# Kernel tuning notes

Hardware: AMD Instinct MI355X
Metric: run time of the kernel (lower is better)

Reference implementation:

```python
import jax, jax.numpy as jnp
import numpy as np

B, T, D, H = 16384, 80, 12, 128


def setup_inputs() -> dict:
    key = jax.random.key(0)
    ks = jax.random.split(key, 20)
    stdv = lambda n: 1.0 / np.sqrt(n)
    u = lambda k, shp, s: jax.random.uniform(k, shp, jnp.float32, -s, s)
    inp = {
        'values': jax.random.normal(ks[0], (B, T, D), jnp.float32),
        'masks': (jax.random.uniform(ks[1], (B, T, D)) < 0.8).astype(jnp.float32),
        'deltas': jax.random.uniform(ks[2], (B, T, D), jnp.float32, 0.0, 5.0),
        'td_h_W': u(ks[3], (H, D), stdv(H)), 'td_h_b': u(ks[4], (H,), stdv(H)),
        'td_x_W': u(ks[5], (D, D), stdv(D)), 'td_x_b': u(ks[6], (D,), stdv(D)),
        'hist_W': u(ks[7], (D, H), stdv(H)), 'hist_b': u(ks[8], (D,), stdv(H)),
        'feat_W': u(ks[9], (D, D), stdv(D)), 'feat_b': u(ks[10], (D,), stdv(D)),
        'wc_W': u(ks[11], (D, 2 * D), stdv(2 * D)), 'wc_b': u(ks[12], (D,), stdv(2 * D)),
        'W_ih': u(ks[13], (4 * H, 2 * D), stdv(H)), 'b_ih': u(ks[14], (4 * H,), stdv(H)),
        'W_hh': u(ks[15], (4 * H, H), stdv(H)), 'b_hh': u(ks[16], (4 * H,), stdv(H)),
        'out_W': u(ks[17], (1, H), stdv(H)), 'out_b': u(ks[18], (1,), stdv(H)),
    }
    return inp


def _forward(values, masks, deltas, td_h_W, td_h_b, td_x_W, td_x_b,
             hist_W, hist_b, feat_W, feat_b, wc_W, wc_b,
             W_ih, b_ih, W_hh, b_hh, out_W, out_b):
    eye = jnp.eye(D, dtype=values.dtype)
    td_x_Wd = td_x_W * eye            # diagonal temporal decay
    feat_Wm = feat_W * (1.0 - eye)

    xs = (jnp.swapaxes(values, 0, 1),  # [T,B,D]
          jnp.swapaxes(masks, 0, 1),
          jnp.swapaxes(deltas, 0, 1))

    def step(carry, xmd):
        h, c, x_loss = carry
        x, m, d = xmd
        gamma_h = jnp.exp(-jax.nn.relu(d @ td_h_W.T + td_h_b))   # [B,H]
        gamma_x = jnp.exp(-jax.nn.relu(d @ td_x_Wd.T + td_x_b))  # [B,D]
        h = h * gamma_h
        x_h = h @ hist_W.T + hist_b
        denom = jnp.sum(m) + 1e-5
        x_loss += jnp.sum(jnp.abs(x - x_h) * m) / denom
        x_c = m * x + (1.0 - m) * x_h
        z_h = x_c @ feat_Wm.T + feat_b
        x_loss += jnp.sum(jnp.abs(x - z_h) * m) / denom
        alpha = jnp.concatenate([gamma_x, m], axis=1) @ wc_W.T + wc_b
        c_h = alpha * z_h + (1.0 - alpha) * x_h
        x_loss += jnp.sum(jnp.abs(x - c_h) * m) / denom
        c_c = m * x + (1.0 - m) * c_h
        inp = jnp.concatenate([c_c, m], axis=1)                  # [B,2D]
        gates = inp @ W_ih.T + b_ih + h @ W_hh.T + b_hh          # [B,4H]
        i, f, g, o = jnp.split(gates, 4, axis=1)
        c = jax.nn.sigmoid(f) * c + jax.nn.sigmoid(i) * jnp.tanh(g)
        h = jax.nn.sigmoid(o) * jnp.tanh(c)
        return (h, c, x_loss), c_c

    h0 = jnp.zeros((values.shape[0], H), values.dtype)
    c0 = jnp.zeros((values.shape[0], H), values.dtype)
    (h, c, x_loss), imps = jax.lax.scan(step, (h0, c0, jnp.float32(0.0)), xs)
    loss = x_loss / T
    predictions = jax.nn.sigmoid(h @ out_W.T + out_b)            # [B,1]
    imputations = jnp.swapaxes(imps, 0, 1)                       # [B,T,D]
    return loss, predictions, imputations


def reference(values, masks, deltas, td_h_W, td_h_b, td_x_W, td_x_b,
              hist_W, hist_b, feat_W, feat_b, wc_W, wc_b,
              W_ih, b_ih, W_hh, b_hh, out_W, out_b):
    return _forward(values, masks, deltas, td_h_W, td_h_b, td_x_W, td_x_b,
                    hist_W, hist_b, feat_W, feat_b, wc_W, wc_b,
                    W_ih, b_ih, W_hh, b_hh, out_W, out_b)
```

## Files before the change

### kernel.cpp

```cpp
#include <hip/hip_runtime.h>

#define B_ 16384
#define T_ 80
#define D_ 12
#define H_ 128
#define BT 32
#define NTH 512
#define NBLK (B_ / BT)

#define NLOG2E -1.4426950408889634f
#define TWOLOG2E 2.8853900817779268f

typedef unsigned short us_t;
typedef unsigned int u32_t;
typedef short bf16x8 __attribute__((ext_vector_type(8)));
typedef float f32x4 __attribute__((ext_vector_type(4)));

__device__ __forceinline__ us_t f2bf_bit(float f){
  u32_t x = __float_as_uint(f);
  return (us_t)((x + 0x7FFFu + ((x >> 16) & 1u)) >> 16);
}
__device__ __forceinline__ us_t f2bf(float f){
  u32_t r;
  asm("v_cvt_pk_bf16_f32 %0, %1, %2" : "=v"(r) : "v"(f), "v"(f));
  return (us_t)r;
}
__device__ __forceinline__ float bf2f(us_t u){
  union { u32_t i; float f; } v; v.i = ((u32_t)u) << 16; return v.f;
}
__device__ __forceinline__ float rcpf(float x){ return __builtin_amdgcn_rcpf(x); }
#if __has_builtin(__builtin_amdgcn_exp2f)
__device__ __forceinline__ float exp2f_(float x){ return __builtin_amdgcn_exp2f(x); }
#else
__device__ __forceinline__ float exp2f_(float x){ return __expf(0.6931471805599453f * x); }
#endif
__device__ __forceinline__ float sigm(float x){ return rcpf(1.f + __expf(-x)); }

__global__ void k_denom(const float* __restrict__ masks, float* __restrict__ denomInv) {
  int t = blockIdx.x, tid = threadIdx.x;
  float s = 0.f;
  for (int b = tid; b < B_; b += 256) {
    const float4* p = (const float4*)(masks + ((size_t)b * T_ + t) * D_);
    float4 a = p[0], c = p[1], d = p[2];
    s += a.x + a.y + a.z + a.w + c.x + c.y + c.z + c.w + d.x + d.y + d.z + d.w;
  }
  __shared__ float r[256];
  r[tid] = s; __syncthreads();
  for (int st = 128; st > 0; st >>= 1) { if (tid < st) r[tid] += r[tid + st]; __syncthreads(); }
  if (tid == 0) denomInv[t] = 1.f / (r[0] + 1e-5f);
}

__global__ void k_pack(const float* __restrict__ W_ih, const float* __restrict__ W_hh,
                       const float* __restrict__ hist_W, const float* __restrict__ td_h_W,
                       const float* __restrict__ b_ih, const float* __restrict__ b_hh,
                       const float* __restrict__ wc_W,
                       us_t* __restrict__ Wb, us_t* __restrict__ histB,
                       us_t* __restrict__ tdhwB, float* __restrict__ bias_pk,
                       us_t* __restrict__ wcB) {
  int idx = blockIdx.x * 256 + threadIdx.x;
  if (idx < 81920) {
    int i = idx & 7, lane = (idx >> 3) & 63, rest = idx >> 9;
    int kc = rest % 5; rest /= 5;
    int g = rest & 3, w = rest >> 2;
    int n = g * 128 + w * 16 + (lane & 15);
    int k = kc * 32 + ((lane >> 4) << 3) + i;
    float v = 0.f;
    if (k < 24) v = W_ih[n * 24 + k];
    else if (k < 152) v = W_hh[n * 128 + (k - 24)];
    float s = (g == 2) ? TWOLOG2E : NLOG2E;
    Wb[idx] = f2bf_bit(v * s);
  } else if (idx < 83968) {
    int e = idx - 81920;
    int i = e & 7, lane = (e >> 3) & 63, kc = e >> 9;
    int col = lane & 15, k = kc * 32 + ((lane >> 4) << 3) + i;
    histB[e] = f2bf_bit(col < 12 ? hist_W[col * 128 + k] : 0.f);
  } else if (idx < 88064) {
    int e = idx - 83968;
    int i = e & 7, lane = (e >> 3) & 63, w = e >> 9;
    int n = w * 16 + (lane & 15), k = ((lane >> 4) << 3) + i;
    tdhwB[e] = f2bf_bit(k < 12 ? td_h_W[n * 12 + k] * NLOG2E : 0.f);
  } else if (idx < 88576) {
    int e = idx - 88064;
    int g = e >> 7;
    float s = (g == 2) ? TWOLOG2E : NLOG2E;
    bias_pk[e] = (b_ih[e] + b_hh[e]) * s;
  } else if (idx < 89088) {
    int e = idx - 88576;
    int i = e & 7, lane = e >> 3;
    int col = lane & 15, k = ((lane >> 4) << 3) + i;
    wcB[e] = f2bf_bit((col < 12 && k < 24) ? wc_W[col * 24 + k] : 0.f);
  }
}

#define STAGE_WRITE(BUF, V) do { \
  if (la == 0) { \
    x_s[BUF][lb][lq*4+0] = (V).x; x_s[BUF][lb][lq*4+1] = (V).y; \
    x_s[BUF][lb][lq*4+2] = (V).z; x_s[BUF][lb][lq*4+3] = (V).w; \
  } else if (la == 1) { \
    m_s[BUF][lb][lq*4+0] = (V).x; m_s[BUF][lb][lq*4+1] = (V).y; \
    m_s[BUF][lb][lq*4+2] = (V).z; m_s[BUF][lb][lq*4+3] = (V).w; \
    float _mv[4] = {(V).x,(V).y,(V).z,(V).w}; \
    _Pragma("unroll") \
    for (int _j = 0; _j < 4; ++_j) { \
      int _k = 12 + lq*4 + _j; \
      us_t _mb = f2bf(_mv[_j]); \
      A_s[BUF][_k>>3][lb][_k&7] = _mb; \
      aA_s[_k>>3][lb][_k&7] = _mb; \
    } \
  } else { \
    float _dv[4] = {(V).x,(V).y,(V).z,(V).w}; \
    _Pragma("unroll") \
    for (int _j = 0; _j < 4; ++_j) { \
      int _i = lq*4+_j; \
      float _gx = exp2f_(fminf(fmaf(_dv[_j], tdxd_s[_i], tdxb_s[_i]), 0.f)); \
      aA_s[_i>>3][lb][_i&7] = f2bf(_gx); \
      dA_s[_i>>3][lb][_i&7] = f2bf(_dv[_j]); \
    } \
  } \
} while(0)

__global__ __launch_bounds__(NTH) void k_main(
    const float* __restrict__ values, const float* __restrict__ masks, const float* __restrict__ deltas,
    const float* __restrict__ td_h_b, const float* __restrict__ td_x_W, const float* __restrict__ td_x_b,
    const float* __restrict__ hist_b, const float* __restrict__ feat_W, const float* __restrict__ feat_b,
    const float* __restrict__ wc_b,
    const float* __restrict__ out_W, const float* __restrict__ out_b,
    const float* __restrict__ denomInv, const float* __restrict__ bias_pk,
    const us_t* __restrict__ Wb, const us_t* __restrict__ histB, const us_t* __restrict__ tdhwB,
    const us_t* __restrict__ wcB,
    float* __restrict__ blockLoss, float* __restrict__ out_pred, float* __restrict__ out_imp) {

  __shared__ __align__(16) us_t A_s[2][20][BT][8];
  __shared__ __align__(16) us_t dA_s[4][BT][8];
  __shared__ __align__(16) us_t aA_s[4][BT][8];
  __shared__ __align__(16) us_t histB_s[4][64][8];
  __shared__ float x_s[2][BT][13], m_s[2][BT][13];
  __shared__ float cct_s[BT][13], xh_s[BT][13], al_s[BT][13];
  __shared__ float featW_s[12][12];
  __shared__ float featb_s[12], tdxd_s[12], tdxb_s[12];
  __shared__ float outW_s[128];
  __shared__ float denomInv_s[80];
  __shared__ float outb_s;
  __shared__ float red_s[NTH];

  const int tid = threadIdx.x;
  const int bs = blockIdx.x * BT;
  const int w = tid >> 6, l = tid & 63;
  const int lr = l & 15, lg = l >> 4;

  for (int i = tid; i < 144; i += NTH)
    featW_s[i / 12][i % 12] = ((i / 12) == (i % 12)) ? 0.f : feat_W[i];
  if (tid < 12) {
    featb_s[tid] = feat_b[tid];
    tdxd_s[tid] = td_x_W[tid * 12 + tid] * NLOG2E;
    tdxb_s[tid] = td_x_b[tid] * NLOG2E;
  }
  if (tid < 128) outW_s[tid] = out_W[tid];
  if (tid < 80) denomInv_s[tid] = denomInv[tid];
  if (tid == 0) outb_s = out_b[0];
  for (int i = tid; i < 2 * 20 * BT * 8; i += NTH) ((us_t*)A_s)[i] = 0;
  for (int i = tid; i < 4 * BT * 8; i += NTH) { ((us_t*)dA_s)[i] = 0; ((us_t*)aA_s)[i] = 0; }
  for (int i = tid; i < 2048; i += NTH) ((us_t*)histB_s)[i] = histB[i];

  bf16x8 bq[4][5];
  #pragma unroll
  for (int g = 0; g < 4; ++g)
    #pragma unroll
    for (int kc = 0; kc < 5; ++kc)
      bq[g][kc] = *(const bf16x8*)(Wb + (size_t)((((w * 4 + g) * 5 + kc) * 64 + l) << 3));
  const bf16x8 twf = *(const bf16x8*)(tdhwB + (size_t)(((w * 64) + l) << 3));
  const bf16x8 wcf = *(const bf16x8*)(wcB + (size_t)(l << 3));
  float bjs[4];
  #pragma unroll
  for (int g = 0; g < 4; ++g) bjs[g] = bias_pk[g * 128 + w * 16 + lr];
  const float tdhb_j = td_h_b[w * 16 + lr] * NLOG2E;
  const float hbias = hist_b[lr < 12 ? lr : 0];
  const float wcb_lr = (lr < 12) ? wc_b[lr] : 0.f;

  const int lt = tid - 192;
  const bool isLoader = (lt >= 0 && lt < 288);
  const int la = isLoader ? lt / 96 : 0;
  const int lrm = isLoader ? lt % 96 : 0;
  const int lb = lrm / 3, lq = lrm % 3;
  const float* lsrc = (la == 0) ? values : (la == 1) ? masks : deltas;

  float c_st[2][4] = {{0.f,0.f,0.f,0.f},{0.f,0.f,0.f,0.f}};
  float lossAcc = 0.f;
  int cur = 0;
  __syncthreads();

  if (isLoader) {
    float4 pv = *(const float4*)(lsrc + ((size_t)(bs + lb) * T_) * D_ + lq * 4);
    STAGE_WRITE(0, pv);
  }
  __syncthreads();

  for (int t = 0; t < T_; ++t) {
    const float dInv = denomInv_s[t];
    const int nxt = cur ^ 1;
    float4 ldv;

    if (w < 2) {
      f32x4 xacc = {0.f, 0.f, 0.f, 0.f};
      #pragma unroll
      for (int kc = 0; kc < 4; ++kc) {
        const bf16x8 af = *(const bf16x8*)&A_s[cur][3 + kc * 4 + lg][w * 16 + lr][0];
        const bf16x8 hf = *(const bf16x8*)&histB_s[kc][l][0];
        xacc = __builtin_amdgcn_mfma_f32_16x16x32_bf16(af, hf, xacc, 0, 0, 0);
      }
      if (lr < 12) {
        #pragma unroll
        for (int r = 0; r < 4; ++r) xh_s[w * 16 + lg * 4 + r][lr] = xacc[r] + hbias;
      }
    } else if (w == 2) {
      f32x4 ac0 = {wcb_lr, wcb_lr, wcb_lr, wcb_lr};
      f32x4 ac1 = ac0;
      const bf16x8 a0 = *(const bf16x8*)&aA_s[lg][lr][0];
      const bf16x8 a1 = *(const bf16x8*)&aA_s[lg][16 + lr][0];
      ac0 = __builtin_amdgcn_mfma_f32_16x16x32_bf16(a0, wcf, ac0, 0, 0, 0);
      ac1 = __builtin_amdgcn_mfma_f32_16x16x32_bf16(a1, wcf, ac1, 0, 0, 0);
      if (lr < 12) {
        #pragma unroll
        for (int r = 0; r < 4; ++r) {
          al_s[lg * 4 + r][lr] = ac0[r];
          al_s[16 + lg * 4 + r][lr] = ac1[r];
        }
      }
    } else if (isLoader) {
      if (t + 1 < T_)
        ldv = *(const float4*)(lsrc + ((size_t)(bs + lb) * T_ + (t + 1)) * D_ + lq * 4);
    } else if (t > 0) {
      int ib = tid - 480;
      #pragma unroll
      for (int q = 0; q < 3; ++q) {
        float4 v = make_float4(cct_s[ib][q * 4 + 0], cct_s[ib][q * 4 + 1],
                               cct_s[ib][q * 4 + 2], cct_s[ib][q * 4 + 3]);
        *(float4*)(out_imp + ((size_t)(bs + ib) * T_ + (t - 1)) * D_ + q * 4) = v;
      }
    }
    __syncthreads();

    if (isLoader && (t + 1 < T_)) STAGE_WRITE(nxt, ldv);
    if (tid < 384) {
      int b = tid & 31, i = tid >> 5;
      float xh = xh_s[b][i], xv = x_s[cur][b][i], mv = m_s[cur][b][i];
      float es = fabsf(xv - xh) * mv;
      float zh = featb_s[i];
      #pragma unroll
      for (int k = 0; k < 12; ++k) {
        float xck = fmaf(m_s[cur][b][k], x_s[cur][b][k] - xh_s[b][k], xh_s[b][k]);
        zh = fmaf(xck, featW_s[i][k], zh);
      }
      es += fabsf(xv - zh) * mv;
      float al = al_s[b][i];
      float ch = fmaf(al, zh - xh, xh);
      es += fabsf(xv - ch) * mv;
      lossAcc = fmaf(es, dInv, lossAcc);
      float cc = fmaf(mv, xv - ch, ch);
      cct_s[b][i] = cc;
      A_s[cur][i >> 3][b][i & 7] = f2bf(cc);
    }
    __syncthreads();

    {
      f32x4 acc[2][4];
      #pragma unroll
      for (int m = 0; m < 2; ++m)
        #pragma unroll
        for (int g = 0; g < 4; ++g)
          acc[m][g] = (f32x4){bjs[g], bjs[g], bjs[g], bjs[g]};
      __builtin_amdgcn_s_setprio(1);
      #pragma unroll
      for (int kc = 0; kc < 5; ++kc) {
        const bf16x8 a0 = *(const bf16x8*)&A_s[cur][kc * 4 + lg][lr][0];
        const bf16x8 a1 = *(const bf16x8*)&A_s[cur][kc * 4 + lg][16 + lr][0];
        #pragma unroll
        for (int g = 0; g < 4; ++g) {
          acc[0][g] = __builtin_amdgcn_mfma_f32_16x16x32_bf16(a0, bq[g][kc], acc[0][g], 0, 0, 0);
          acc[1][g] = __builtin_amdgcn_mfma_f32_16x16x32_bf16(a1, bq[g][kc], acc[1][g], 0, 0, 0);
        }
      }
      f32x4 g0 = {tdhb_j, tdhb_j, tdhb_j, tdhb_j};
      f32x4 g1 = g0;
      const bf16x8 d0 = *(const bf16x8*)&dA_s[lg][lr][0];
      const bf16x8 d1 = *(const bf16x8*)&dA_s[lg][16 + lr][0];
      g0 = __builtin_amdgcn_mfma_f32_16x16x32_bf16(d0, twf, g0, 0, 0, 0);
      g1 = __builtin_amdgcn_mfma_f32_16x16x32_bf16(d1, twf, g1, 0, 0, 0);
      __builtin_amdgcn_s_setprio(0);
      const bool dec = (t + 1 < T_);
      const int kgh = 3 + 2 * w + (lr >> 3), pgh = lr & 7;
      #pragma unroll
      for (int m = 0; m < 2; ++m) {
        #pragma unroll
        for (int r = 0; r < 4; ++r) {
          float gi = rcpf(1.f + exp2f_(acc[m][0][r]));
          float gf = rcpf(1.f + exp2f_(acc[m][1][r]));
          float gg = 1.f - 2.f * rcpf(1.f + exp2f_(acc[m][2][r]));
          float go = rcpf(1.f + exp2f_(acc[m][3][r]));
          float c = fmaf(gf, c_st[m][r], gi * gg);
          c_st[m][r] = c;
          float th = 1.f - 2.f * rcpf(1.f + exp2f_(TWOLOG2E * c));
          float pre = (m == 0 ? g0[r] : g1[r]);
          float gh = dec ? exp2f_(fminf(pre, 0.f)) : 1.f;
          A_s[nxt][kgh][m * 16 + lg * 4 + r][pgh] = f2bf(go * th * gh);
        }
      }
    }
    __syncthreads();
    cur = nxt;
  }

  if (tid >= 480) {
    int ib = tid - 480;
    #pragma unroll
    for (int q = 0; q < 3; ++q) {
      float4 v = make_float4(cct_s[ib][q * 4 + 0], cct_s[ib][q * 4 + 1],
                             cct_s[ib][q * 4 + 2], cct_s[ib][q * 4 + 3]);
      *(float4*)(out_imp + ((size_t)(bs + ib) * T_ + (T_ - 1)) * D_ + q * 4) = v;
    }
  }

  if (tid < BT) {
    float a = outb_s;
    #pragma unroll 4
    for (int k = 0; k < H_; ++k)
      a = fmaf(bf2f(A_s[cur][3 + (k >> 3)][tid][k & 7]), outW_s[k], a);
    out_pred[bs + tid] = sigm(a);
  }

  red_s[tid] = lossAcc;
  __syncthreads();
  for (int s = NTH / 2; s > 0; s >>= 1) { if (tid < s) red_s[tid] += red_s[tid + s]; __syncthreads(); }
  if (tid == 0) blockLoss[blockIdx.x] = red_s[0];
}

__global__ void k_final(const float* __restrict__ blockLoss, float* __restrict__ out_loss) {
  __shared__ float r[256];
  int tid = threadIdx.x;
  r[tid] = blockLoss[tid] + blockLoss[tid + 256];
  __syncthreads();
  for (int s = 128; s > 0; s >>= 1) { if (tid < s) r[tid] += r[tid + s]; __syncthreads(); }
  if (tid == 0) out_loss[0] = r[0] * (1.f / (float)T_);
}

extern "C" void kernel_launch(void* const* d_in, const int* in_sizes, int n_in,
                              void* d_out, int out_size, void* d_ws, size_t ws_size,
                              hipStream_t stream) {
  const float* values = (const float*)d_in[0];
  const float* masks  = (const float*)d_in[1];
  const float* deltas = (const float*)d_in[2];
  const float* td_h_W = (const float*)d_in[3];
  const float* td_h_b = (const float*)d_in[4];
  const float* td_x_W = (const float*)d_in[5];
  const float* td_x_b = (const float*)d_in[6];
  const float* hist_W = (const float*)d_in[7];
  const float* hist_b = (const float*)d_in[8];
  const float* feat_W = (const float*)d_in[9];
  const float* feat_b = (const float*)d_in[10];
  const float* wc_W   = (const float*)d_in[11];
  const float* wc_b   = (const float*)d_in[12];
  const float* W_ih   = (const float*)d_in[13];
  const float* b_ih   = (const float*)d_in[14];
  const float* W_hh   = (const float*)d_in[15];
  const float* b_hh   = (const float*)d_in[16];
  const float* out_W  = (const float*)d_in[17];
  const float* out_b  = (const float*)d_in[18];

  float* ws_f      = (float*)d_ws;
  float* denomInv  = ws_f;
  float* bias_pk   = ws_f + 128;
  float* blockLoss = ws_f + 1024;
  us_t* Wb    = (us_t*)(ws_f + 2048);
  us_t* histB = Wb + 81920;
  us_t* tdhwB = histB + 2048;
  us_t* wcB   = tdhwB + 4096;

  float* out_f = (float*)d_out;

  k_denom<<<T_, 256, 0, stream>>>(masks, denomInv);
  k_pack<<<348, 256, 0, stream>>>(W_ih, W_hh, hist_W, td_h_W, b_ih, b_hh, wc_W,
                                  Wb, histB, tdhwB, bias_pk, wcB);
  k_main<<<NBLK, NTH, 0, stream>>>(values, masks, deltas, td_h_b, td_x_W, td_x_b,
                                   hist_b, feat_W, feat_b, wc_b,
                                   out_W, out_b, denomInv, bias_pk, Wb, histB, tdhwB, wcB,
                                   blockLoss, out_f + 1, out_f + 1 + B_);
  k_final<<<1, 256, 0, stream>>>(blockLoss, out_f);
}
```

Baseline: 458.5 us.

## Process two 32-row batch tiles per block to amortize per-step syncs

Doubles the batch tile from 32 to 64 rows per block by giving every shared-memory buffer and the cell state a tile dimension, then looping each pipeline stage over the two 32-row sub-tiles. This halves the grid to 256 blocks and spreads the per-timestep barrier and weight-register setup over twice the work. The cost is fewer blocks than CUs on a 256-CU part, longer serial work per step, and more shared memory and registers, which can lower occupancy. The final loss reduction is adjusted to read 256 block partials.

```diff
diff --git a/kernel.cpp b/kernel.cpp
--- a/kernel.cpp
+++ b/kernel.cpp
@@ -4,7 +4,7 @@
 #define T_ 80
 #define D_ 12
 #define H_ 128
-#define BT 32
+#define BT 64
 #define NTH 512
 #define NBLK (B_ / BT)
 
@@ -92,20 +92,20 @@
   }
 }
 
-#define STAGE_WRITE(BUF, V) do { \
+#define STAGE_WRITE(TL, BUF, V) do { \
   if (la == 0) { \
-    x_s[BUF][lb][lq*4+0] = (V).x; x_s[BUF][lb][lq*4+1] = (V).y; \
-    x_s[BUF][lb][lq*4+2] = (V).z; x_s[BUF][lb][lq*4+3] = (V).w; \
+    x_s[TL][BUF][lb][lq*4+0] = (V).x; x_s[TL][BUF][lb][lq*4+1] = (V).y; \
+    x_s[TL][BUF][lb][lq*4+2] = (V).z; x_s[TL][BUF][lb][lq*4+3] = (V).w; \
   } else if (la == 1) { \
-    m_s[BUF][lb][lq*4+0] = (V).x; m_s[BUF][lb][lq*4+1] = (V).y; \
-    m_s[BUF][lb][lq*4+2] = (V).z; m_s[BUF][lb][lq*4+3] = (V).w; \
+    m_s[TL][BUF][lb][lq*4+0] = (V).x; m_s[TL][BUF][lb][lq*4+1] = (V).y; \
+    m_s[TL][BUF][lb][lq*4+2] = (V).z; m_s[TL][BUF][lb][lq*4+3] = (V).w; \
     float _mv[4] = {(V).x,(V).y,(V).z,(V).w}; \
     _Pragma("unroll") \
     for (int _j = 0; _j < 4; ++_j) { \
       int _k = 12 + lq*4 + _j; \
       us_t _mb = f2bf(_mv[_j]); \
-      A_s[BUF][_k>>3][lb][_k&7] = _mb; \
-      aA_s[_k>>3][lb][_k&7] = _mb; \
+      A_s[TL][BUF][_k>>3][lb][_k&7] = _mb; \
+      aA_s[TL][_k>>3][lb][_k&7] = _mb; \
     } \
   } else { \
     float _dv[4] = {(V).x,(V).y,(V).z,(V).w}; \
@@ -113,8 +113,8 @@
     for (int _j = 0; _j < 4; ++_j) { \
       int _i = lq*4+_j; \
       float _gx = exp2f_(fminf(fmaf(_dv[_j], tdxd_s[_i], tdxb_s[_i]), 0.f)); \
-      aA_s[_i>>3][lb][_i&7] = f2bf(_gx); \
-      dA_s[_i>>3][lb][_i&7] = f2bf(_dv[_j]); \
+      aA_s[TL][_i>>3][lb][_i&7] = f2bf(_gx); \
+      dA_s[TL][_i>>3][lb][_i&7] = f2bf(_dv[_j]); \
     } \
   } \
 } while(0)
@@ -130,12 +130,12 @@
     const us_t* __restrict__ wcB,
     float* __restrict__ blockLoss, float* __restrict__ out_pred, float* __restrict__ out_imp) {
 
-  __shared__ __align__(16) us_t A_s[2][20][BT][8];
-  __shared__ __align__(16) us_t dA_s[4][BT][8];
-  __shared__ __align__(16) us_t aA_s[4][BT][8];
+  __shared__ __align__(16) us_t A_s[2][2][20][32][8];
+  __shared__ __align__(16) us_t dA_s[2][4][32][8];
+  __shared__ __align__(16) us_t aA_s[2][4][32][8];
   __shared__ __align__(16) us_t histB_s[4][64][8];
-  __shared__ float x_s[2][BT][13], m_s[2][BT][13];
-  __shared__ float cct_s[BT][13], xh_s[BT][13], al_s[BT][13];
+  __shared__ float x_s[2][2][32][13], m_s[2][2][32][13];
+  __shared__ float cct_s[2][32][13], xh_s[2][32][13], al_s[2][32][13];
   __shared__ float featW_s[12][12];
   __shared__ float featb_s[12], tdxd_s[12], tdxb_s[12];
   __shared__ float outW_s[128];
@@ -158,8 +158,8 @@
   if (tid < 128) outW_s[tid] = out_W[tid];
   if (tid < 80) denomInv_s[tid] = denomInv[tid];
   if (tid == 0) outb_s = out_b[0];
-  for (int i = tid; i < 2 * 20 * BT * 8; i += NTH) ((us_t*)A_s)[i] = 0;
-  for (int i = tid; i < 4 * BT * 8; i += NTH) { ((us_t*)dA_s)[i] = 0; ((us_t*)aA_s)[i] = 0; }
+  for (int i = tid; i < 2 * 2 * 20 * 32 * 8; i += NTH) ((us_t*)A_s)[i] = 0;
+  for (int i = tid; i < 2 * 4 * 32 * 8; i += NTH) { ((us_t*)dA_s)[i] = 0; ((us_t*)aA_s)[i] = 0; }
   for (int i = tid; i < 2048; i += NTH) ((us_t*)histB_s)[i] = histB[i];
 
   bf16x8 bq[4][5];
@@ -184,85 +184,107 @@
   const int lb = lrm / 3, lq = lrm % 3;
   const float* lsrc = (la == 0) ? values : (la == 1) ? masks : deltas;
 
-  float c_st[2][4] = {{0.f,0.f,0.f,0.f},{0.f,0.f,0.f,0.f}};
+  float c_st[2][2][4];
+  #pragma unroll
+  for (int tl = 0; tl < 2; ++tl)
+    #pragma unroll
+    for (int m = 0; m < 2; ++m)
+      #pragma unroll
+      for (int r = 0; r < 4; ++r) c_st[tl][m][r] = 0.f;
   float lossAcc = 0.f;
   int cur = 0;
   __syncthreads();
 
   if (isLoader) {
-    float4 pv = *(const float4*)(lsrc + ((size_t)(bs + lb) * T_) * D_ + lq * 4);
-    STAGE_WRITE(0, pv);
+    float4 p0 = *(const float4*)(lsrc + ((size_t)(bs + lb) * T_) * D_ + lq * 4);
+    float4 p1 = *(const float4*)(lsrc + ((size_t)(bs + 32 + lb) * T_) * D_ + lq * 4);
+    STAGE_WRITE(0, 0, p0);
+    STAGE_WRITE(1, 0, p1);
   }
   __syncthreads();
 
   for (int t = 0; t < T_; ++t) {
     const float dInv = denomInv_s[t];
     const int nxt = cur ^ 1;
-    float4 ldv;
+    float4 ldv0, ldv1;
 
     if (w < 2) {
-      f32x4 xacc = {0.f, 0.f, 0.f, 0.f};
-      #pragma unroll
-      for (int kc = 0; kc < 4; ++kc) {
-        const bf16x8 af = *(const bf16x8*)&A_s[cur][3 + kc * 4 + lg][w * 16 + lr][0];
-        const bf16x8 hf = *(const bf16x8*)&histB_s[kc][l][0];
-        xacc = __builtin_amdgcn_mfma_f32_16x16x32_bf16(af, hf, xacc, 0, 0, 0);
-      }
-      if (lr < 12) {
-        #pragma unroll
-        for (int r = 0; r < 4; ++r) xh_s[w * 16 + lg * 4 + r][lr] = xacc[r] + hbias;
+      #pragma unroll
+      for (int tl = 0; tl < 2; ++tl) {
+        f32x4 xacc = {0.f, 0.f, 0.f, 0.f};
+        #pragma unroll
+        for (int kc = 0; kc < 4; ++kc) {
+          const bf16x8 af = *(const bf16x8*)&A_s[tl][cur][3 + kc * 4 + lg][w * 16 + lr][0];
+          const bf16x8 hf = *(const bf16x8*)&histB_s[kc][l][0];
+          xacc = __builtin_amdgcn_mfma_f32_16x16x32_bf16(af, hf, xacc, 0, 0, 0);
+        }
+        if (lr < 12) {
+          #pragma unroll
+          for (int r = 0; r < 4; ++r) xh_s[tl][w * 16 + lg * 4 + r][lr] = xacc[r] + hbias;
+        }
       }
     } else if (w == 2) {
-      f32x4 ac0 = {wcb_lr, wcb_lr, wcb_lr, wcb_lr};
-      f32x4 ac1 = ac0;
-      const bf16x8 a0 = *(const bf16x8*)&aA_s[lg][lr][0];
-      const bf16x8 a1 = *(const bf16x8*)&aA_s[lg][16 + lr][0];
-      ac0 = __builtin_amdgcn_mfma_f32_16x16x32_bf16(a0, wcf, ac0, 0, 0, 0);
-      ac1 = __builtin_amdgcn_mfma_f32_16x16x32_bf16(a1, wcf, ac1, 0, 0, 0);
-      if (lr < 12) {
-        #pragma unroll
-        for (int r = 0; r < 4; ++r) {
-          al_s[lg * 4 + r][lr] = ac0[r];
-          al_s[16 + lg * 4 + r][lr] = ac1[r];
+      #pragma unroll
+      for (int tl = 0; tl < 2; ++tl) {
+        f32x4 ac0 = {wcb_lr, wcb_lr, wcb_lr, wcb_lr};
+        f32x4 ac1 = ac0;
+        const bf16x8 a0 = *(const bf16x8*)&aA_s[tl][lg][lr][0];
+        const bf16x8 a1 = *(const bf16x8*)&aA_s[tl][lg][16 + lr][0];
+        ac0 = __builtin_amdgcn_mfma_f32_16x16x32_bf16(a0, wcf, ac0, 0, 0, 0);
+        ac1 = __builtin_amdgcn_mfma_f32_16x16x32_bf16(a1, wcf, ac1, 0, 0, 0);
+        if (lr < 12) {
+          #pragma unroll
+          for (int r = 0; r < 4; ++r) {
+            al_s[tl][lg * 4 + r][lr] = ac0[r];
+            al_s[tl][16 + lg * 4 + r][lr] = ac1[r];
+          }
         }
       }
     } else if (isLoader) {
-      if (t + 1 < T_)
-        ldv = *(const float4*)(lsrc + ((size_t)(bs + lb) * T_ + (t + 1)) * D_ + lq * 4);
+      if (t + 1 < T_) {
+        ldv0 = *(const float4*)(lsrc + ((size_t)(bs + lb) * T_ + (t + 1)) * D_ + lq * 4);
+        ldv1 = *(const float4*)(lsrc + ((size_t)(bs + 32 + lb) * T_ + (t + 1)) * D_ + lq * 4);
+      }
     } else if (t > 0) {
       int ib = tid - 480;
       #pragma unroll
-      for (int q = 0; q < 3; ++q) {
-        float4 v = make_float4(cct_s[ib][q * 4 + 0], cct_s[ib][q * 4 + 1],
-                               cct_s[ib][q * 4 + 2], cct_s[ib][q * 4 + 3]);
-        *(float4*)(out_imp + ((size_t)(bs + ib) * T_ + (t - 1)) * D_ + q * 4) = v;
-      }
+      for (int tl = 0; tl < 2; ++tl)
+        #pragma unroll
+        for (int q = 0; q < 3; ++q) {
+          float4 v = make_float4(cct_s[tl][ib][q * 4 + 0], cct_s[tl][ib][q * 4 + 1],
+                                 cct_s[tl][ib][q * 4 + 2], cct_s[tl][ib][q * 4 + 3]);
+          *(float4*)(out_imp + ((size_t)(bs + tl * 32 + ib) * T_ + (t - 1)) * D_ + q * 4) = v;
+        }
     }
     __syncthreads();
 
-    if (isLoader && (t + 1 < T_)) STAGE_WRITE(nxt, ldv);
+    if (isLoader && (t + 1 < T_)) { STAGE_WRITE(0, nxt, ldv0); STAGE_WRITE(1, nxt, ldv1); }
     if (tid < 384) {
-      int b = tid & 31, i = tid >> 5;
-      float xh = xh_s[b][i], xv = x_s[cur][b][i], mv = m_s[cur][b][i];
-      float es = fabsf(xv - xh) * mv;
-      float zh = featb_s[i];
-      #pragma unroll
-      for (int k = 0; k < 12; ++k) {
-        float xck = fmaf(m_s[cur][b][k], x_s[cur][b][k] - xh_s[b][k], xh_s[b][k]);
-        zh = fmaf(xck, featW_s[i][k], zh);
-      }
-      es += fabsf(xv - zh) * mv;
-      float al = al_s[b][i];
-      float ch = fmaf(al, zh - xh, xh);
-      es += fabsf(xv - ch) * mv;
-      lossAcc = fmaf(es, dInv, lossAcc);
-      float cc = fmaf(mv, xv - ch, ch);
-      cct_s[b][i] = cc;
-      A_s[cur][i >> 3][b][i & 7] = f2bf(cc);
+      #pragma unroll
+      for (int tl = 0; tl < 2; ++tl) {
+        int b = tid & 31, i = tid >> 5;
+        float xh = xh_s[tl][b][i], xv = x_s[tl][cur][b][i], mv = m_s[tl][cur][b][i];
+        float es = fabsf(xv - xh) * mv;
+        float zh = featb_s[i];
+        #pragma unroll
+        for (int k = 0; k < 12; ++k) {
+          float xck = fmaf(m_s[tl][cur][b][k], x_s[tl][cur][b][k] - xh_s[tl][b][k], xh_s[tl][b][k]);
+          zh = fmaf(xck, featW_s[i][k], zh);
+        }
+        es += fabsf(xv - zh) * mv;
+        float al = al_s[tl][b][i];
+        float ch = fmaf(al, zh - xh, xh);
+        es += fabsf(xv - ch) * mv;
+        lossAcc = fmaf(es, dInv, lossAcc);
+        float cc = fmaf(mv, xv - ch, ch);
+        cct_s[tl][b][i] = cc;
+        A_s[tl][cur][i >> 3][b][i & 7] = f2bf(cc);
+      }
     }
     __syncthreads();
 
-    {
+    #pragma unroll
+    for (int tl = 0; tl < 2; ++tl) {
       f32x4 acc[2][4];
       #pragma unroll
       for (int m = 0; m < 2; ++m)
@@ -272,8 +294,8 @@
       __builtin_amdgcn_s_setprio(1);
       #pragma unroll
       for (int kc = 0; kc < 5; ++kc) {
-        const bf16x8 a0 = *(const bf16x8*)&A_s[cur][kc * 4 + lg][lr][0];
-        const bf16x8 a1 = *(const bf16x8*)&A_s[cur][kc * 4 + lg][16 + lr][0];
+        const bf16x8 a0 = *(const bf16x8*)&A_s[tl][cur][kc * 4 + lg][lr][0];
+        const bf16x8 a1 = *(const bf16x8*)&A_s[tl][cur][kc * 4 + lg][16 + lr][0];
         #pragma unroll
         for (int g = 0; g < 4; ++g) {
           acc[0][g] = __builtin_amdgcn_mfma_f32_16x16x32_bf16(a0, bq[g][kc], acc[0][g], 0, 0, 0);
@@ -282,8 +304,8 @@
       }
       f32x4 g0 = {tdhb_j, tdhb_j, tdhb_j, tdhb_j};
       f32x4 g1 = g0;
-      const bf16x8 d0 = *(const bf16x8*)&dA_s[lg][lr][0];
-      const bf16x8 d1 = *(const bf16x8*)&dA_s[lg][16 + lr][0];
+      const bf16x8 d0 = *(const bf16x8*)&dA_s[tl][lg][lr][0];
+      const bf16x8 d1 = *(const bf16x8*)&dA_s[tl][lg][16 + lr][0];
       g0 = __builtin_amdgcn_mfma_f32_16x16x32_bf16(d0, twf, g0, 0, 0, 0);
       g1 = __builtin_amdgcn_mfma_f32_16x16x32_bf16(d1, twf, g1, 0, 0, 0);
       __builtin_amdgcn_s_setprio(0);
@@ -297,12 +319,12 @@
           float gf = rcpf(1.f + exp2f_(acc[m][1][r]));
           float gg = 1.f - 2.f * rcpf(1.f + exp2f_(acc[m][2][r]));
           float go = rcpf(1.f + exp2f_(acc[m][3][r]));
-          float c = fmaf(gf, c_st[m][r], gi * gg);
-          c_st[m][r] = c;
+          float c = fmaf(gf, c_st[tl][m][r], gi * gg);
+          c_st[tl][m][r] = c;
           float th = 1.f - 2.f * rcpf(1.f + exp2f_(TWOLOG2E * c));
           float pre = (m == 0 ? g0[r] : g1[r]);
           float gh = dec ? exp2f_(fminf(pre, 0.f)) : 1.f;
-          A_s[nxt][kgh][m * 16 + lg * 4 + r][pgh] = f2bf(go * th * gh);
+          A_s[tl][nxt][kgh][m * 16 + lg * 4 + r][pgh] = f2bf(go * th * gh);
         }
       }
     }
@@ -313,19 +335,22 @@
   if (tid >= 480) {
     int ib = tid - 480;
     #pragma unroll
-    for (int q = 0; q < 3; ++q) {
-      float4 v = make_float4(cct_s[ib][q * 4 + 0], cct_s[ib][q * 4 + 1],
-                             cct_s[ib][q * 4 + 2], cct_s[ib][q * 4 + 3]);
-      *(float4*)(out_imp + ((size_t)(bs + ib) * T_ + (T_ - 1)) * D_ + q * 4) = v;
-    }
+    for (int tl = 0; tl < 2; ++tl)
+      #pragma unroll
+      for (int q = 0; q < 3; ++q) {
+        float4 v = make_float4(cct_s[tl][ib][q * 4 + 0], cct_s[tl][ib][q * 4 + 1],
+                               cct_s[tl][ib][q * 4 + 2], cct_s[tl][ib][q * 4 + 3]);
+        *(float4*)(out_imp + ((size_t)(bs + tl * 32 + ib) * T_ + (T_ - 1)) * D_ + q * 4) = v;
+      }
   }
 
   if (tid < BT) {
+    int tl = tid >> 5, b = tid & 31;
     float a = outb_s;
     #pragma unroll 4
     for (int k = 0; k < H_; ++k)
-      a = fmaf(bf2f(A_s[cur][3 + (k >> 3)][tid][k & 7]), outW_s[k], a);
-    out_pred[bs + tid] = sigm(a);
+      a = fmaf(bf2f(A_s[tl][cur][3 + (k >> 3)][b][k & 7]), outW_s[k], a);
+    out_pred[bs + tl * 32 + b] = sigm(a);
   }
 
   red_s[tid] = lossAcc;
@@ -337,7 +362,7 @@
 __global__ void k_final(const float* __restrict__ blockLoss, float* __restrict__ out_loss) {
   __shared__ float r[256];
   int tid = threadIdx.x;
-  r[tid] = blockLoss[tid] + blockLoss[tid + 256];
+  r[tid] = blockLoss[tid];
   __syncthreads();
   for (int s = 128; s > 0; s >>= 1) { if (tid < s) r[tid] += r[tid + s]; __syncthreads(); }
   if (tid == 0) out_loss[0] = r[0] * (1.f / (float)T_);
```

After: 448.9 us, median of 2. -2.1%, faster.
